# Kernel tuning notes

Hardware: AMD Instinct MI355X
Metric: run time of the kernel (lower is better)

## Reference

```python
import jax, jax.numpy as jnp
import numpy as np

T = 14        # num_tokens per image dimension
H_HEADS = 12  # attention heads
D = 768       # d_model
FF = 3072     # ff_dim


def setup_inputs() -> dict:
    key = jax.random.key(0)
    ks = jax.random.split(key, 5)
    s = 0.02
    return {
        "x": jax.random.normal(ks[0], (4, D, 224, 224), dtype=jnp.float32),
        "w_in": jax.random.normal(ks[1], (3 * D, D), dtype=jnp.float32) * s,
        "b_in": jnp.zeros((3 * D,), dtype=jnp.float32),
        "w_out": jax.random.normal(ks[2], (D, D), dtype=jnp.float32) * s,
        "b_out": jnp.zeros((D,), dtype=jnp.float32),
        "w_fc1": jax.random.normal(ks[3], (FF, D), dtype=jnp.float32) * s,
        "b_fc1": jnp.zeros((FF,), dtype=jnp.float32),
        "w_fc2": jax.random.normal(ks[4], (D, FF), dtype=jnp.float32) * s,
        "b_fc2": jnp.zeros((D,), dtype=jnp.float32),
    }


def _atm_forward(x, w_in, b_in, w_out, b_out, w_fc1, b_fc1, w_fc2, b_fc2):
    B, d, W, Hh = x.shape
    g = Hh // T                      # grid_size
    L = g * g                        # tokens per grid cell (after raw reshape)
    N = T * T                        # number of grid cells / queries
    hd = d // H_HEADS                # head dim

    # Query: adaptive avg pool to (T, T) == mean over g x g blocks
    xg = x.reshape(B, d, T, g, T, g)
    q = xg.mean(axis=(3, 5))                     # [B, d, T, T]
    q = q.reshape(B, d, N).transpose(0, 2, 1)    # [B, N, d]

    # Key/Value: faithful replication of unfold().view(x.size()).reshape(B,-1,d):
    # [B,T,T,d,g,g] flat-reinterpreted so each cell's (d,g,g) slab -> (g*g, d) rows.
    kv6 = xg.transpose(0, 2, 4, 1, 3, 5)         # [B, T, T, d, g, g]
    kv = kv6.reshape(B, N, L, d)                 # block-diagonal KV per grid cell

    # Batched multi-head cross attention: 1 query per block vs L keys per block
    wq, wk, wv = w_in[:D], w_in[D:2 * D], w_in[2 * D:]
    bq, bk, bv = b_in[:D], b_in[D:2 * D], b_in[2 * D:]
    qp = (q @ wq.T + bq).reshape(B, N, H_HEADS, hd)          # [B,N,h,hd]
    kp = (kv @ wk.T + bk).reshape(B, N, L, H_HEADS, hd)      # [B,N,L,h,hd]
    vp = (kv @ wv.T + bv).reshape(B, N, L, H_HEADS, hd)

    scale = 1.0 / jnp.sqrt(jnp.asarray(hd, dtype=x.dtype))
    scores = jnp.einsum('bnhc,bnlhc->bnhl', qp, kp) * scale  # [B,N,h,L]
    attn = jax.nn.softmax(scores, axis=-1)
    ctx = jnp.einsum('bnhl,bnlhc->bnhc', attn, vp)           # [B,N,h,hd]
    out = ctx.reshape(B, N, d) @ w_out.T + b_out             # [B,N,d]

    # FeedForwardNetwork (dropout = eval / identity)
    h1 = out @ w_fc1.T + b_fc1
    h1 = jax.nn.silu(h1)
    y = h1 @ w_fc2.T + b_fc2
    return y


def reference(x, w_in, b_in, w_out, b_out, w_fc1, b_fc1, w_fc2, b_fc2):
    return _atm_forward(x, w_in, b_in, w_out, b_out, w_fc1, b_fc1, w_fc2, b_fc2)
```

## Files before the change

### kernel.cpp

```cpp
#include <hip/hip_runtime.h>

#define B_   4
#define T_   14
#define N_   196
#define D_   768
#define NH   12
#define HD   64
#define LL   256
#define FF_  3072
#define IMG  224
#define CHW  (IMG*IMG)
#define BN   (B_*N_)

__global__ __launch_bounds__(256) void pool_kernel(const float* __restrict__ x,
                                                   float* __restrict__ q) {
    int blk = blockIdx.x;
    int b = blk / N_, n = blk % N_;
    int t1 = n / T_, t2 = n % T_;
    const float* xb = x + (size_t)b * D_ * CHW + (size_t)(t1 * 16) * IMG + t2 * 16;
    float* qb = q + (size_t)blk * D_;

    int tid = threadIdx.x;
    int w = tid >> 6, lane = tid & 63;
    int g1 = lane >> 2, g2b = lane & 3;

    for (int c = w; c < D_; c += 4) {
        const float* p = xb + (size_t)c * CHW + g1 * IMG + g2b * 4;
        float4 v = *reinterpret_cast<const float4*>(p);
        float s = v.x + v.y + v.z + v.w;
        #pragma unroll
        for (int off = 32; off > 0; off >>= 1) s += __shfl_xor(s, off);
        if (lane == 0) qb[c] = s * (1.0f / 256.0f);
    }
}

template <int TRANSW, int ACT>
__global__ __launch_bounds__(256) void gemm_kernel(
    const float* __restrict__ A, const float* __restrict__ W,
    const float* __restrict__ bias, float* __restrict__ C,
    int M, int N, int K, int lda, int ldw, int ldc,
    long azs, long wzs, long czs, int bzs) {

    A += (long)blockIdx.z * azs;
    W += (long)blockIdx.z * wzs;
    C += (long)blockIdx.z * czs;
    if (bias) bias += (long)blockIdx.z * bzs;

    __shared__ float As[16][68];
    __shared__ float Ws[16][68];

    int tid = threadIdx.x;
    int m0 = blockIdx.x * 64, n0 = blockIdx.y * 64;
    int tx = tid & 15, ty = tid >> 4;

    float acc[4][4] = {};

    for (int k0 = 0; k0 < K; k0 += 16) {
        {
            int m = tid >> 2;
            int kk = (tid & 3) * 4;
            int gm = m0 + m;
            float4 a = make_float4(0.f, 0.f, 0.f, 0.f);
            if (gm < M) a = *reinterpret_cast<const float4*>(&A[(size_t)gm * lda + k0 + kk]);
            As[kk + 0][m] = a.x; As[kk + 1][m] = a.y;
            As[kk + 2][m] = a.z; As[kk + 3][m] = a.w;
        }
        if (TRANSW) {
            int nn = tid >> 2;
            int kk = (tid & 3) * 4;
            float4 v = *reinterpret_cast<const float4*>(&W[(size_t)(n0 + nn) * ldw + k0 + kk]);
            Ws[kk + 0][nn] = v.x; Ws[kk + 1][nn] = v.y;
            Ws[kk + 2][nn] = v.z; Ws[kk + 3][nn] = v.w;
        } else {
            int kk = tid >> 4;
            int nn = (tid & 15) * 4;
            float4 v = *reinterpret_cast<const float4*>(&W[(size_t)(k0 + kk) * ldw + n0 + nn]);
            Ws[kk][nn + 0] = v.x; Ws[kk][nn + 1] = v.y;
            Ws[kk][nn + 2] = v.z; Ws[kk][nn + 3] = v.w;
        }
        __syncthreads();

        #pragma unroll
        for (int kk = 0; kk < 16; ++kk) {
            float4 a = *reinterpret_cast<const float4*>(&As[kk][ty * 4]);
            float4 b = *reinterpret_cast<const float4*>(&Ws[kk][tx * 4]);
            acc[0][0] += a.x * b.x; acc[0][1] += a.x * b.y; acc[0][2] += a.x * b.z; acc[0][3] += a.x * b.w;
            acc[1][0] += a.y * b.x; acc[1][1] += a.y * b.y; acc[1][2] += a.y * b.z; acc[1][3] += a.y * b.w;
            acc[2][0] += a.z * b.x; acc[2][1] += a.z * b.y; acc[2][2] += a.z * b.z; acc[2][3] += a.z * b.w;
            acc[3][0] += a.w * b.x; acc[3][1] += a.w * b.y; acc[3][2] += a.w * b.z; acc[3][3] += a.w * b.w;
        }
        __syncthreads();
    }

    float4 bv = make_float4(0.f, 0.f, 0.f, 0.f);
    if (bias) bv = *reinterpret_cast<const float4*>(&bias[n0 + tx * 4]);

    #pragma unroll
    for (int i = 0; i < 4; ++i) {
        int gm = m0 + ty * 4 + i;
        if (gm >= M) continue;
        float4 o;
        o.x = acc[i][0] + bv.x; o.y = acc[i][1] + bv.y;
        o.z = acc[i][2] + bv.z; o.w = acc[i][3] + bv.w;
        if (ACT) {
            o.x = o.x / (1.f + __expf(-o.x));
            o.y = o.y / (1.f + __expf(-o.y));
            o.z = o.z / (1.f + __expf(-o.z));
            o.w = o.w / (1.f + __expf(-o.w));
        }
        *reinterpret_cast<float4*>(&C[(size_t)gm * ldc + n0 + tx * 4]) = o;
    }
}

__global__ __launch_bounds__(512) void attn_kernel(const float* __restrict__ x,
                                                   const float* __restrict__ qk,
                                                   float* __restrict__ wkv) {
    int blk = blockIdx.x;
    int b = blk / N_, n = blk % N_;
    int t1 = n / T_, t2 = n % T_;
    const float* xb = x + (size_t)b * D_ * CHW + (size_t)(t1 * 16) * IMG + t2 * 16;
    const float* qkb = qk + (size_t)blk * (NH * D_);
    float* wkvb = wkv + (size_t)blk * (NH * D_);

    __shared__ float qk_s[NH * D_];
    __shared__ float p_s[NH][LL];
    __shared__ float p2_s[NH][LL];
    __shared__ float invsum_s[NH];

    int tid = threadIdx.x;
    int w = tid >> 6, lane = tid & 63;

    for (int i = tid; i < NH * D_ / 4; i += 512)
        reinterpret_cast<float4*>(qk_s)[i] = reinterpret_cast<const float4*>(qkb)[i];
    __syncthreads();

    {
        int l = (w & 3) * 64 + lane;
        int ch = w >> 2;
        float acc[NH];
        #pragma unroll
        for (int h = 0; h < NH; ++h) acc[h] = 0.f;
        const float* xl = xb + (size_t)(3 * l) * CHW;

        for (int co = 0; co < 3; ++co) {
            const float* xc = xl + (size_t)co * CHW;
            for (int g1 = ch * 8; g1 < ch * 8 + 8; ++g1) {
                const float* row = xc + g1 * IMG;
                #pragma unroll
                for (int g2b = 0; g2b < 4; ++g2b) {
                    float4 kv = *reinterpret_cast<const float4*>(row + g2b * 4);
                    int cc = co * 256 + g1 * 16 + g2b * 4;
                    #pragma unroll
                    for (int h = 0; h < NH; ++h) {
                        float4 qv = *reinterpret_cast<const float4*>(&qk_s[h * D_ + cc]);
                        acc[h] += qv.x * kv.x + qv.y * kv.y + qv.z * kv.z + qv.w * kv.w;
                    }
                }
            }
        }
        float* dst = ch ? &p2_s[0][0] : &p_s[0][0];
        #pragma unroll
        for (int h = 0; h < NH; ++h) dst[h * LL + l] = acc[h];
    }
    __syncthreads();

    const float scale = 0.125f;
    for (int h = w; h < NH; h += 8) {
        float v[4];
        float mx = -1e30f;
        #pragma unroll
        for (int j = 0; j < 4; ++j) {
            int l = lane + 64 * j;
            v[j] = (p_s[h][l] + p2_s[h][l]) * scale;
            mx = fmaxf(mx, v[j]);
        }
        #pragma unroll
        for (int off = 32; off > 0; off >>= 1) mx = fmaxf(mx, __shfl_xor(mx, off));
        float sum = 0.f;
        #pragma unroll
        for (int j = 0; j < 4; ++j) { v[j] = __expf(v[j] - mx); sum += v[j]; }
        #pragma unroll
        for (int off = 32; off > 0; off >>= 1) sum += __shfl_xor(sum, off);
        #pragma unroll
        for (int j = 0; j < 4; ++j) p_s[h][lane + 64 * j] = v[j];
        if (lane == 0) invsum_s[h] = 1.0f / sum;
    }
    __syncthreads();

    {
        int hg = w & 3;
        int r = w >> 2;
        float4 acc[3][3];
        #pragma unroll
        for (int hh = 0; hh < 3; ++hh)
            #pragma unroll
            for (int f = 0; f < 3; ++f) acc[hh][f] = make_float4(0.f, 0.f, 0.f, 0.f);

        int g1 = lane >> 2, g2b = lane & 3;
        for (int l = r * 128; l < r * 128 + 128; ++l) {
            const float* xl = xb + (size_t)(3 * l) * CHW + g1 * IMG + g2b * 4;
            float p0 = p_s[hg * 3 + 0][l];
            float p1 = p_s[hg * 3 + 1][l];
            float p2v = p_s[hg * 3 + 2][l];
            #pragma unroll
            for (int f = 0; f < 3; ++f) {
                float4 kv = *reinterpret_cast<const float4*>(xl + (size_t)f * CHW);
                acc[0][f].x += p0 * kv.x;  acc[0][f].y += p0 * kv.y;
                acc[0][f].z += p0 * kv.z;  acc[0][f].w += p0 * kv.w;
                acc[1][f].x += p1 * kv.x;  acc[1][f].y += p1 * kv.y;
                acc[1][f].z += p1 * kv.z;  acc[1][f].w += p1 * kv.w;
                acc[2][f].x += p2v * kv.x; acc[2][f].y += p2v * kv.y;
                acc[2][f].z += p2v * kv.z; acc[2][f].w += p2v * kv.w;
            }
        }

        float* stg = qk_s;
        int slot = lane * 4;
        if (r == 0) {
            #pragma unroll
            for (int hh = 0; hh < 3; ++hh)
                #pragma unroll
                for (int f = 0; f < 3; ++f)
                    *reinterpret_cast<float4*>(&stg[(hg * 3 + hh) * D_ + f * 256 + slot]) = acc[hh][f];
        }
        __syncthreads();
        if (r == 1) {
            #pragma unroll
            for (int hh = 0; hh < 3; ++hh) {
                float inv = invsum_s[hg * 3 + hh];
                #pragma unroll
                for (int f = 0; f < 3; ++f) {
                    float4 o = *reinterpret_cast<float4*>(&stg[(hg * 3 + hh) * D_ + f * 256 + slot]);
                    float4 s;
                    s.x = (acc[hh][f].x + o.x) * inv;
                    s.y = (acc[hh][f].y + o.y) * inv;
                    s.z = (acc[hh][f].z + o.z) * inv;
                    s.w = (acc[hh][f].w + o.w) * inv;
                    *reinterpret_cast<float4*>(&wkvb[(hg * 3 + hh) * D_ + f * 256 + slot]) = s;
                }
            }
        }
    }
}

extern "C" void kernel_launch(void* const* d_in, const int* in_sizes, int n_in,
                              void* d_out, int out_size, void* d_ws, size_t ws_size,
                              hipStream_t stream) {
    const float* x     = (const float*)d_in[0];
    const float* w_in  = (const float*)d_in[1];
    const float* b_in  = (const float*)d_in[2];
    const float* w_out = (const float*)d_in[3];
    const float* b_out = (const float*)d_in[4];
    const float* w_fc1 = (const float*)d_in[5];
    const float* b_fc1 = (const float*)d_in[6];
    const float* w_fc2 = (const float*)d_in[7];
    const float* b_fc2 = (const float*)d_in[8];
    float* y = (float*)d_out;

    float* ws   = (float*)d_ws;
    float* q    = ws;
    float* qp   = q    + (size_t)BN * D_;
    float* qkb  = qp   + (size_t)BN * D_;
    float* wkv  = qkb  + (size_t)BN * NH * D_;
    float* ctx  = wkv  + (size_t)BN * NH * D_;
    float* aout = ctx  + (size_t)BN * D_;
    float* h1   = aout + (size_t)BN * D_;

    const float* wq = w_in;
    const float* wk = w_in + (size_t)D_ * D_;
    const float* wv = w_in + (size_t)2 * D_ * D_;
    const float* bq = b_in;
    const float* bv = b_in + 2 * D_;

    pool_kernel<<<dim3(BN), dim3(256), 0, stream>>>(x, q);

    gemm_kernel<1, 0><<<dim3(13, 12, 1), dim3(256), 0, stream>>>(
        q, wq, bq, qp, BN, D_, D_, D_, D_, D_, 0, 0, 0, 0);

    gemm_kernel<0, 0><<<dim3(13, 12, NH), dim3(256), 0, stream>>>(
        qp, wk, nullptr, qkb, BN, D_, HD, D_, D_, NH * D_,
        (long)HD, (long)HD * D_, (long)D_, 0);

    attn_kernel<<<dim3(BN), dim3(512), 0, stream>>>(x, qkb, wkv);

    gemm_kernel<1, 0><<<dim3(13, 1, NH), dim3(256), 0, stream>>>(
        wkv, wv, bv, ctx, BN, HD, D_, NH * D_, D_, D_,
        (long)D_, (long)HD * D_, (long)HD, HD);

    gemm_kernel<1, 0><<<dim3(13, 12, 1), dim3(256), 0, stream>>>(
        ctx, w_out, b_out, aout, BN, D_, D_, D_, D_, D_, 0, 0, 0, 0);

    gemm_kernel<1, 1><<<dim3(13, 48, 1), dim3(256), 0, stream>>>(
        aout, w_fc1, b_fc1, h1, BN, FF_, D_, D_, D_, FF_, 0, 0, 0, 0);

    gemm_kernel<1, 0><<<dim3(13, 12, 1), dim3(256), 0, stream>>>(
        h1, w_fc2, b_fc2, y, BN, D_, FF_, FF_, FF_, D_, 0, 0, 0, 0);
}
```

Measured before the change: 1.751 ms.

## Add split-K GEMMs, rework pooling layout, and tile attention with online softmax

The pool kernel now gives each block a row of grid cells and a slice of channels, so each wave reads full contiguous image rows instead of 16-wide strips. The small GEMMs (q projection, V projection, out projection, fc2) are split along K into partial-sum buffers, followed by a reduction kernel that adds the bias, so more blocks are launched. The attention kernel processes the 256 keys in tiles of 64 with an online softmax and reads each key row as four float4s. In exchange there are extra launches and partial-sum traffic, and the partial buffers reuse the h1 and qkb workspace regions.

```diff
diff --git a/kernel.cpp b/kernel.cpp
--- a/kernel.cpp
+++ b/kernel.cpp
@@ -7,6 +7,7 @@
 #define NH   12
 #define HD   64
 #define LL   256
+#define LT   64
 #define FF_  3072
 #define IMG  224
 #define CHW  (IMG*IMG)
@@ -15,22 +16,33 @@
 __global__ __launch_bounds__(256) void pool_kernel(const float* __restrict__ x,
                                                    float* __restrict__ q) {
     int blk = blockIdx.x;
-    int b = blk / N_, n = blk % N_;
-    int t1 = n / T_, t2 = n % T_;
-    const float* xb = x + (size_t)b * D_ * CHW + (size_t)(t1 * 16) * IMG + t2 * 16;
-    float* qb = q + (size_t)blk * D_;
-
+    int cs = blk & 15;
+    int bt = blk >> 4;
+    int t1 = bt % T_, b = bt / T_;
     int tid = threadIdx.x;
     int w = tid >> 6, lane = tid & 63;
-    int g1 = lane >> 2, g2b = lane & 3;
-
-    for (int c = w; c < D_; c += 4) {
-        const float* p = xb + (size_t)c * CHW + g1 * IMG + g2b * 4;
-        float4 v = *reinterpret_cast<const float4*>(p);
-        float s = v.x + v.y + v.z + v.w;
-        #pragma unroll
-        for (int off = 32; off > 0; off >>= 1) s += __shfl_xor(s, off);
-        if (lane == 0) qb[c] = s * (1.0f / 256.0f);
+    bool act = lane < 56;
+    int t2 = lane >> 2;
+
+    const float* xb = x + (size_t)b * D_ * CHW + (size_t)(t1 * 16) * IMG;
+
+    #pragma unroll 2
+    for (int i = 0; i < 12; ++i) {
+        int c = cs * 48 + w * 12 + i;
+        const float* xc = xb + (size_t)c * CHW;
+        float acc = 0.f;
+        for (int g1 = 0; g1 < 16; ++g1) {
+            float s = 0.f;
+            if (act) {
+                float4 v = *reinterpret_cast<const float4*>(xc + g1 * IMG + lane * 4);
+                s = v.x + v.y + v.z + v.w;
+            }
+            s += __shfl_xor(s, 1);
+            s += __shfl_xor(s, 2);
+            acc += s;
+        }
+        if (act && (lane & 3) == 0)
+            q[((size_t)b * N_ + t1 * T_ + t2) * D_ + c] = acc * (1.0f / 256.0f);
     }
 }
 
@@ -38,13 +50,18 @@
 __global__ __launch_bounds__(256) void gemm_kernel(
     const float* __restrict__ A, const float* __restrict__ W,
     const float* __restrict__ bias, float* __restrict__ C,
+    float* __restrict__ Cpart,
     int M, int N, int K, int lda, int ldw, int ldc,
-    long azs, long wzs, long czs, int bzs) {
-
-    A += (long)blockIdx.z * azs;
-    W += (long)blockIdx.z * wzs;
-    C += (long)blockIdx.z * czs;
-    if (bias) bias += (long)blockIdx.z * bzs;
+    long azs, long wzs, long czs, int bzs, int KS) {
+
+    int gz = blockIdx.z;
+    int ks = gz % KS, zb = gz / KS;
+    A += (long)zb * azs;
+    W += (long)zb * wzs;
+    if (bias) bias += (long)zb * bzs;
+
+    int kbeg = ks * (K / KS);
+    int kend = kbeg + K / KS;
 
     __shared__ float As[16][68];
     __shared__ float Ws[16][68];
@@ -55,7 +72,7 @@
 
     float acc[4][4] = {};
 
-    for (int k0 = 0; k0 < K; k0 += 16) {
+    for (int k0 = kbeg; k0 < kend; k0 += 16) {
         {
             int m = tid >> 2;
             int kk = (tid & 3) * 4;
@@ -92,29 +109,72 @@
         __syncthreads();
     }
 
-    float4 bv = make_float4(0.f, 0.f, 0.f, 0.f);
-    if (bias) bv = *reinterpret_cast<const float4*>(&bias[n0 + tx * 4]);
-
-    #pragma unroll
-    for (int i = 0; i < 4; ++i) {
-        int gm = m0 + ty * 4 + i;
-        if (gm >= M) continue;
-        float4 o;
-        o.x = acc[i][0] + bv.x; o.y = acc[i][1] + bv.y;
-        o.z = acc[i][2] + bv.z; o.w = acc[i][3] + bv.w;
-        if (ACT) {
-            o.x = o.x / (1.f + __expf(-o.x));
-            o.y = o.y / (1.f + __expf(-o.y));
-            o.z = o.z / (1.f + __expf(-o.z));
-            o.w = o.w / (1.f + __expf(-o.w));
-        }
-        *reinterpret_cast<float4*>(&C[(size_t)gm * ldc + n0 + tx * 4]) = o;
-    }
-}
-
-__global__ __launch_bounds__(512) void attn_kernel(const float* __restrict__ x,
-                                                   const float* __restrict__ qk,
-                                                   float* __restrict__ wkv) {
+    if (KS == 1) {
+        float4 bv = make_float4(0.f, 0.f, 0.f, 0.f);
+        if (bias) bv = *reinterpret_cast<const float4*>(&bias[n0 + tx * 4]);
+        #pragma unroll
+        for (int i = 0; i < 4; ++i) {
+            int gm = m0 + ty * 4 + i;
+            if (gm >= M) continue;
+            float4 o;
+            o.x = acc[i][0] + bv.x; o.y = acc[i][1] + bv.y;
+            o.z = acc[i][2] + bv.z; o.w = acc[i][3] + bv.w;
+            if (ACT) {
+                o.x = o.x / (1.f + __expf(-o.x));
+                o.y = o.y / (1.f + __expf(-o.y));
+                o.z = o.z / (1.f + __expf(-o.z));
+                o.w = o.w / (1.f + __expf(-o.w));
+            }
+            *reinterpret_cast<float4*>(&C[(long)zb * czs + (size_t)gm * ldc + n0 + tx * 4]) = o;
+        }
+    } else {
+        #pragma unroll
+        for (int i = 0; i < 4; ++i) {
+            int gm = m0 + ty * 4 + i;
+            if (gm >= M) continue;
+            float4 o = make_float4(acc[i][0], acc[i][1], acc[i][2], acc[i][3]);
+            *reinterpret_cast<float4*>(
+                &Cpart[(((long)zb * KS + ks) * M + gm) * N + n0 + tx * 4]) = o;
+        }
+    }
+}
+
+template <int ACT>
+__global__ __launch_bounds__(256) void fix_kernel(
+    const float* __restrict__ P, const float* __restrict__ bias,
+    float* __restrict__ C, int M, int N, int ldc, long czs, int bzs,
+    int KS, int Z) {
+
+    int gid = blockIdx.x * 256 + threadIdx.x;
+    int per_z = M * (N >> 2);
+    if (gid >= Z * per_z) return;
+    int zb = gid / per_z;
+    int rem = gid - zb * per_z;
+    int m = rem / (N >> 2);
+    int n4 = (rem - m * (N >> 2)) << 2;
+
+    float4 s = make_float4(0.f, 0.f, 0.f, 0.f);
+    for (int ks = 0; ks < KS; ++ks) {
+        float4 v = *reinterpret_cast<const float4*>(
+            &P[(((long)zb * KS + ks) * M + m) * N + n4]);
+        s.x += v.x; s.y += v.y; s.z += v.z; s.w += v.w;
+    }
+    if (bias) {
+        float4 bv = *reinterpret_cast<const float4*>(&bias[zb * bzs + n4]);
+        s.x += bv.x; s.y += bv.y; s.z += bv.z; s.w += bv.w;
+    }
+    if (ACT) {
+        s.x = s.x / (1.f + __expf(-s.x));
+        s.y = s.y / (1.f + __expf(-s.y));
+        s.z = s.z / (1.f + __expf(-s.z));
+        s.w = s.w / (1.f + __expf(-s.w));
+    }
+    *reinterpret_cast<float4*>(&C[(long)zb * czs + (long)m * ldc + n4]) = s;
+}
+
+__global__ __launch_bounds__(512, 4) void attn_kernel(const float* __restrict__ x,
+                                                      const float* __restrict__ qk,
+                                                      float* __restrict__ wkv) {
     int blk = blockIdx.x;
     int b = blk / N_, n = blk % N_;
     int t1 = n / T_, t2 = n % T_;
@@ -123,121 +183,134 @@
     float* wkvb = wkv + (size_t)blk * (NH * D_);
 
     __shared__ float qk_s[NH * D_];
-    __shared__ float p_s[NH][LL];
-    __shared__ float p2_s[NH][LL];
-    __shared__ float invsum_s[NH];
+    __shared__ float pp[8][NH][LT];
+    __shared__ float p_s[NH][LT];
+    __shared__ float m_s[NH], s_s[NH], f_s[NH];
 
     int tid = threadIdx.x;
     int w = tid >> 6, lane = tid & 63;
 
     for (int i = tid; i < NH * D_ / 4; i += 512)
         reinterpret_cast<float4*>(qk_s)[i] = reinterpret_cast<const float4*>(qkb)[i];
+    if (tid < NH) { m_s[tid] = -1e30f; s_s[tid] = 0.f; }
+
+    int hg = w & 3, r = w >> 2;
+    int g1b = lane >> 2, g2b = lane & 3;
+    float4 oacc[3][3];
+    #pragma unroll
+    for (int hh = 0; hh < 3; ++hh)
+        #pragma unroll
+        for (int co = 0; co < 3; ++co) oacc[hh][co] = make_float4(0.f, 0.f, 0.f, 0.f);
+
     __syncthreads();
 
-    {
-        int l = (w & 3) * 64 + lane;
-        int ch = w >> 2;
-        float acc[NH];
-        #pragma unroll
-        for (int h = 0; h < NH; ++h) acc[h] = 0.f;
-        const float* xl = xb + (size_t)(3 * l) * CHW;
-
-        for (int co = 0; co < 3; ++co) {
-            const float* xc = xl + (size_t)co * CHW;
-            for (int g1 = ch * 8; g1 < ch * 8 + 8; ++g1) {
-                const float* row = xc + g1 * IMG;
-                #pragma unroll
-                for (int g2b = 0; g2b < 4; ++g2b) {
-                    float4 kv = *reinterpret_cast<const float4*>(row + g2b * 4);
-                    int cc = co * 256 + g1 * 16 + g2b * 4;
-                    #pragma unroll
-                    for (int h = 0; h < NH; ++h) {
-                        float4 qv = *reinterpret_cast<const float4*>(&qk_s[h * D_ + cc]);
-                        acc[h] += qv.x * kv.x + qv.y * kv.y + qv.z * kv.z + qv.w * kv.w;
-                    }
-                }
-            }
-        }
-        float* dst = ch ? &p2_s[0][0] : &p_s[0][0];
-        #pragma unroll
-        for (int h = 0; h < NH; ++h) dst[h * LL + l] = acc[h];
-    }
-    __syncthreads();
-
-    const float scale = 0.125f;
-    for (int h = w; h < NH; h += 8) {
-        float v[4];
-        float mx = -1e30f;
-        #pragma unroll
-        for (int j = 0; j < 4; ++j) {
-            int l = lane + 64 * j;
-            v[j] = (p_s[h][l] + p2_s[h][l]) * scale;
-            mx = fmaxf(mx, v[j]);
-        }
-        #pragma unroll
-        for (int off = 32; off > 0; off >>= 1) mx = fmaxf(mx, __shfl_xor(mx, off));
-        float sum = 0.f;
-        #pragma unroll
-        for (int j = 0; j < 4; ++j) { v[j] = __expf(v[j] - mx); sum += v[j]; }
-        #pragma unroll
-        for (int off = 32; off > 0; off >>= 1) sum += __shfl_xor(sum, off);
-        #pragma unroll
-        for (int j = 0; j < 4; ++j) p_s[h][lane + 64 * j] = v[j];
-        if (lane == 0) invsum_s[h] = 1.0f / sum;
-    }
-    __syncthreads();
-
-    {
-        int hg = w & 3;
-        int r = w >> 2;
-        float4 acc[3][3];
+    for (int t = 0; t < LL / LT; ++t) {
+        int lg = t * LT + lane;
+        float acc1[NH];
+        #pragma unroll
+        for (int h = 0; h < NH; ++h) acc1[h] = 0.f;
+
+        #pragma unroll
+        for (int j = 0; j < 6; ++j) {
+            int p = w * 6 + j;
+            int co = p >> 4, g1 = p & 15;
+            const float* rowp = xb + (size_t)(3 * lg + co) * CHW + g1 * IMG;
+            float4 k0 = *reinterpret_cast<const float4*>(rowp + 0);
+            float4 k1 = *reinterpret_cast<const float4*>(rowp + 4);
+            float4 k2 = *reinterpret_cast<const float4*>(rowp + 8);
+            float4 k3 = *reinterpret_cast<const float4*>(rowp + 12);
+            int base = co * 256 + g1 * 16;
+            #pragma unroll
+            for (int h = 0; h < NH; ++h) {
+                const float4* q4 = reinterpret_cast<const float4*>(&qk_s[h * D_ + base]);
+                float4 q0 = q4[0], q1 = q4[1], q2 = q4[2], q3 = q4[3];
+                acc1[h] += q0.x * k0.x + q0.y * k0.y + q0.z * k0.z + q0.w * k0.w
+                         + q1.x * k1.x + q1.y * k1.y + q1.z * k1.z + q1.w * k1.w
+                         + q2.x * k2.x + q2.y * k2.y + q2.z * k2.z + q2.w * k2.w
+                         + q3.x * k3.x + q3.y * k3.y + q3.z * k3.z + q3.w * k3.w;
+            }
+        }
+        #pragma unroll
+        for (int h = 0; h < NH; ++h) pp[w][h][lane] = acc1[h];
+        __syncthreads();
+
+        for (int h = w; h < NH; h += 8) {
+            float s = 0.f;
+            #pragma unroll
+            for (int ww = 0; ww < 8; ++ww) s += pp[ww][h][lane];
+            s *= 0.125f;
+            float mt = s;
+            #pragma unroll
+            for (int off = 32; off > 0; off >>= 1) mt = fmaxf(mt, __shfl_xor(mt, off));
+            float m_old = m_s[h];
+            float m_new = fmaxf(m_old, mt);
+            float e = __expf(s - m_new);
+            float sum = e;
+            #pragma unroll
+            for (int off = 32; off > 0; off >>= 1) sum += __shfl_xor(sum, off);
+            p_s[h][lane] = e;
+            if (lane == 0) {
+                float f = __expf(m_old - m_new);
+                f_s[h] = f;
+                s_s[h] = s_s[h] * f + sum;
+                m_s[h] = m_new;
+            }
+        }
+        __syncthreads();
+
+        float fr[3];
+        fr[0] = f_s[hg * 3 + 0]; fr[1] = f_s[hg * 3 + 1]; fr[2] = f_s[hg * 3 + 2];
         #pragma unroll
         for (int hh = 0; hh < 3; ++hh)
             #pragma unroll
-            for (int f = 0; f < 3; ++f) acc[hh][f] = make_float4(0.f, 0.f, 0.f, 0.f);
-
-        int g1 = lane >> 2, g2b = lane & 3;
-        for (int l = r * 128; l < r * 128 + 128; ++l) {
-            const float* xl = xb + (size_t)(3 * l) * CHW + g1 * IMG + g2b * 4;
+            for (int co = 0; co < 3; ++co) {
+                oacc[hh][co].x *= fr[hh]; oacc[hh][co].y *= fr[hh];
+                oacc[hh][co].z *= fr[hh]; oacc[hh][co].w *= fr[hh];
+            }
+
+        for (int lt = 0; lt < LT / 2; ++lt) {
+            int l = r * (LT / 2) + lt;
+            int lg2 = t * LT + l;
+            const float* xl = xb + (size_t)(3 * lg2) * CHW + g1b * IMG + g2b * 4;
             float p0 = p_s[hg * 3 + 0][l];
             float p1 = p_s[hg * 3 + 1][l];
             float p2v = p_s[hg * 3 + 2][l];
             #pragma unroll
-            for (int f = 0; f < 3; ++f) {
-                float4 kv = *reinterpret_cast<const float4*>(xl + (size_t)f * CHW);
-                acc[0][f].x += p0 * kv.x;  acc[0][f].y += p0 * kv.y;
-                acc[0][f].z += p0 * kv.z;  acc[0][f].w += p0 * kv.w;
-                acc[1][f].x += p1 * kv.x;  acc[1][f].y += p1 * kv.y;
-                acc[1][f].z += p1 * kv.z;  acc[1][f].w += p1 * kv.w;
-                acc[2][f].x += p2v * kv.x; acc[2][f].y += p2v * kv.y;
-                acc[2][f].z += p2v * kv.z; acc[2][f].w += p2v * kv.w;
-            }
-        }
-
-        float* stg = qk_s;
-        int slot = lane * 4;
-        if (r == 0) {
-            #pragma unroll
-            for (int hh = 0; hh < 3; ++hh)
-                #pragma unroll
-                for (int f = 0; f < 3; ++f)
-                    *reinterpret_cast<float4*>(&stg[(hg * 3 + hh) * D_ + f * 256 + slot]) = acc[hh][f];
-        }
-        __syncthreads();
-        if (r == 1) {
-            #pragma unroll
-            for (int hh = 0; hh < 3; ++hh) {
-                float inv = invsum_s[hg * 3 + hh];
-                #pragma unroll
-                for (int f = 0; f < 3; ++f) {
-                    float4 o = *reinterpret_cast<float4*>(&stg[(hg * 3 + hh) * D_ + f * 256 + slot]);
-                    float4 s;
-                    s.x = (acc[hh][f].x + o.x) * inv;
-                    s.y = (acc[hh][f].y + o.y) * inv;
-                    s.z = (acc[hh][f].z + o.z) * inv;
-                    s.w = (acc[hh][f].w + o.w) * inv;
-                    *reinterpret_cast<float4*>(&wkvb[(hg * 3 + hh) * D_ + f * 256 + slot]) = s;
-                }
+            for (int co = 0; co < 3; ++co) {
+                float4 kv = *reinterpret_cast<const float4*>(xl + (size_t)co * CHW);
+                oacc[0][co].x += p0 * kv.x;  oacc[0][co].y += p0 * kv.y;
+                oacc[0][co].z += p0 * kv.z;  oacc[0][co].w += p0 * kv.w;
+                oacc[1][co].x += p1 * kv.x;  oacc[1][co].y += p1 * kv.y;
+                oacc[1][co].z += p1 * kv.z;  oacc[1][co].w += p1 * kv.w;
+                oacc[2][co].x += p2v * kv.x; oacc[2][co].y += p2v * kv.y;
+                oacc[2][co].z += p2v * kv.z; oacc[2][co].w += p2v * kv.w;
+            }
+        }
+        __syncthreads();
+    }
+
+    int slot = lane * 4;
+    if (r == 0) {
+        #pragma unroll
+        for (int hh = 0; hh < 3; ++hh)
+            #pragma unroll
+            for (int co = 0; co < 3; ++co)
+                *reinterpret_cast<float4*>(&qk_s[(hg * 3 + hh) * D_ + co * 256 + slot]) = oacc[hh][co];
+    }
+    __syncthreads();
+    if (r == 1) {
+        #pragma unroll
+        for (int hh = 0; hh < 3; ++hh) {
+            float inv = 1.0f / s_s[hg * 3 + hh];
+            #pragma unroll
+            for (int co = 0; co < 3; ++co) {
+                float4 o = *reinterpret_cast<float4*>(&qk_s[(hg * 3 + hh) * D_ + co * 256 + slot]);
+                float4 s;
+                s.x = (oacc[hh][co].x + o.x) * inv;
+                s.y = (oacc[hh][co].y + o.y) * inv;
+                s.z = (oacc[hh][co].z + o.z) * inv;
+                s.w = (oacc[hh][co].w + o.w) * inv;
+                *reinterpret_cast<float4*>(&wkvb[(hg * 3 + hh) * D_ + co * 256 + slot]) = s;
             }
         }
     }
@@ -266,33 +339,44 @@
     float* aout = ctx  + (size_t)BN * D_;
     float* h1   = aout + (size_t)BN * D_;
 
+    float* pb_h1  = h1;
+    float* pb_qkb = qkb;
+
     const float* wq = w_in;
     const float* wk = w_in + (size_t)D_ * D_;
     const float* wv = w_in + (size_t)2 * D_ * D_;
     const float* bq = b_in;
     const float* bv = b_in + 2 * D_;
 
-    pool_kernel<<<dim3(BN), dim3(256), 0, stream>>>(x, q);
-
-    gemm_kernel<1, 0><<<dim3(13, 12, 1), dim3(256), 0, stream>>>(
-        q, wq, bq, qp, BN, D_, D_, D_, D_, D_, 0, 0, 0, 0);
+    pool_kernel<<<dim3(B_ * T_ * 16), dim3(256), 0, stream>>>(x, q);
+
+    gemm_kernel<1, 0><<<dim3(13, 12, 4), dim3(256), 0, stream>>>(
+        q, wq, nullptr, nullptr, pb_h1, BN, D_, D_, D_, D_, D_, 0, 0, 0, 0, 4);
+    fix_kernel<0><<<dim3(588), dim3(256), 0, stream>>>(
+        pb_h1, bq, qp, BN, D_, D_, 0, 0, 4, 1);
 
     gemm_kernel<0, 0><<<dim3(13, 12, NH), dim3(256), 0, stream>>>(
-        qp, wk, nullptr, qkb, BN, D_, HD, D_, D_, NH * D_,
-        (long)HD, (long)HD * D_, (long)D_, 0);
+        qp, wk, nullptr, qkb, nullptr, BN, D_, HD, D_, D_, NH * D_,
+        (long)HD, (long)HD * D_, (long)D_, 0, 1);
 
     attn_kernel<<<dim3(BN), dim3(512), 0, stream>>>(x, qkb, wkv);
 
-    gemm_kernel<1, 0><<<dim3(13, 1, NH), dim3(256), 0, stream>>>(
-        wkv, wv, bv, ctx, BN, HD, D_, NH * D_, D_, D_,
-        (long)D_, (long)HD * D_, (long)HD, HD);
-
-    gemm_kernel<1, 0><<<dim3(13, 12, 1), dim3(256), 0, stream>>>(
-        ctx, w_out, b_out, aout, BN, D_, D_, D_, D_, D_, 0, 0, 0, 0);
+    gemm_kernel<1, 0><<<dim3(13, 1, NH * 4), dim3(256), 0, stream>>>(
+        wkv, wv, nullptr, nullptr, pb_qkb, BN, HD, D_, NH * D_, D_, D_,
+        (long)D_, (long)HD * D_, (long)HD, HD, 4);
+    fix_kernel<0><<<dim3(588), dim3(256), 0, stream>>>(
+        pb_qkb, bv, ctx, BN, HD, D_, (long)HD, HD, 4, NH);
+
+    gemm_kernel<1, 0><<<dim3(13, 12, 4), dim3(256), 0, stream>>>(
+        ctx, w_out, nullptr, nullptr, pb_qkb, BN, D_, D_, D_, D_, D_, 0, 0, 0, 0, 4);
+    fix_kernel<0><<<dim3(588), dim3(256), 0, stream>>>(
+        pb_qkb, b_out, aout, BN, D_, D_, 0, 0, 4, 1);
 
     gemm_kernel<1, 1><<<dim3(13, 48, 1), dim3(256), 0, stream>>>(
-        aout, w_fc1, b_fc1, h1, BN, FF_, D_, D_, D_, FF_, 0, 0, 0, 0);
-
-    gemm_kernel<1, 0><<<dim3(13, 12, 1), dim3(256), 0, stream>>>(
-        h1, w_fc2, b_fc2, y, BN, D_, FF_, FF_, FF_, D_, 0, 0, 0, 0);
-}
+        aout, w_fc1, b_fc1, h1, nullptr, BN, FF_, D_, D_, D_, FF_, 0, 0, 0, 0, 1);
+
+    gemm_kernel<1, 0><<<dim3(13, 12, 8), dim3(256), 0, stream>>>(
+        h1, w_fc2, nullptr, nullptr, pb_qkb, BN, D_, FF_, FF_, FF_, D_, 0, 0, 0, 0, 8);
+    fix_kernel<0><<<dim3(588), dim3(256), 0, stream>>>(
+        pb_qkb, b_fc2, y, BN, D_, D_, 0, 0, 8, 1);
+}
```

Measured after the change: 1.493 ms. -14.7%, faster.
